# Kernel tuning notes

Hardware: AMD Instinct MI355X
Metric: run time of the kernel (lower is better)

The kernel has to match this reference:

```python
import jax, jax.numpy as jnp
import numpy as np
from jax import lax

B, T, H, W, C = 2, 16, 64, 64, 64
KT, K = 3, 3


def kernel_to_freq_3d(kernel, T, H, W):
    # kernel: (C, k_t, k_h, k_w) -> (C, T, H, W) complex freq response
    Cc, k_t, k_h, k_w = kernel.shape
    t_idx = (jnp.arange(k_t) - k_t // 2) % T
    h_idx = (jnp.arange(k_h) - k_h // 2) % H
    w_idx = (jnp.arange(k_w) - k_w // 2) % W
    tt, th, tw = jnp.meshgrid(t_idx, h_idx, w_idx, indexing='ij')
    padded = jnp.zeros((Cc, T, H, W), dtype=kernel.dtype).at[:, tt, th, tw].set(kernel)
    return jnp.fft.fftn(padded, axes=(1, 2, 3))


def mamba_op(left, right):
    a1, b1 = left
    a2, b2 = right
    return (a1 * a2, a2 * b1 + b2)


def setup_inputs() -> dict:
    key = jax.random.key(0)
    ks = jax.random.split(key, 8)
    fan_in = KT * K * K
    x = jax.random.normal(ks[0], (B, T, H, W, C), dtype=jnp.float32)
    A_kernel = jax.random.normal(ks[1], (C, KT, K, K), dtype=jnp.float32) / np.sqrt(fan_in)
    B_kernel = jax.random.normal(ks[2], (C, KT, K, K), dtype=jnp.float32) / np.sqrt(fan_in)
    forget_bias = jnp.full((C,), 2.0, dtype=jnp.float32)
    forget_scale = jnp.full((C,), 0.01, dtype=jnp.float32)
    input_bias = jnp.zeros((C,), dtype=jnp.float32)
    input_scale = jnp.full((C,), 0.01, dtype=jnp.float32)
    delta_W = jax.random.normal(ks[3], (C, C), dtype=jnp.float32) / np.sqrt(C)
    delta_b = jnp.zeros((C,), dtype=jnp.float32)
    return {"x": x, "A_kernel": A_kernel, "B_kernel": B_kernel,
            "forget_bias": forget_bias, "forget_scale": forget_scale,
            "input_bias": input_bias, "input_scale": input_scale,
            "delta_W": delta_W, "delta_b": delta_b}


def reference(x, A_kernel, B_kernel, forget_bias, forget_scale,
              input_bias, input_scale, delta_W, delta_b):
    Bb, Tt, Hh, Ww, Cc = x.shape
    # freq-domain kernels: (C,T,H,W) -> (T,1,H,W,C) for broadcasting over batch
    A_f = kernel_to_freq_3d(A_kernel, Tt, Hh, Ww).transpose(1, 2, 3, 0)[:, None]
    B_f = kernel_to_freq_3d(B_kernel, Tt, Hh, Ww).transpose(1, 2, 3, 0)[:, None]
    # input-dependent gates (real, elementwise per channel)
    forget_gate = jax.nn.sigmoid(forget_bias + forget_scale * x)
    input_gate = jax.nn.sigmoid(input_bias + input_scale * x)
    delta = jax.nn.softplus(jnp.einsum('bthwc,cd->bthwd', x, delta_W) + delta_b)
    x_f = jnp.fft.fftn(x, axes=(1, 2, 3))  # complex (B,T,H,W,C)
    # move time axis to front for the scan: (T,B,H,W,C)
    a_seq = forget_gate.transpose(1, 0, 2, 3, 4) * A_f
    b_seq = (input_gate.transpose(1, 0, 2, 3, 4)
             * delta.transpose(1, 0, 2, 3, 4)
             * B_f * x_f.transpose(1, 0, 2, 3, 4))
    _, h_all_f = lax.associative_scan(mamba_op, (a_seq, b_seq), axis=0)
    h_f = h_all_f.transpose(1, 0, 2, 3, 4)
    h = jnp.fft.ifftn(h_f, axes=(1, 2, 3)).real
    return h.astype(x.dtype)
```

## Files before the change

### kernel.cpp

```cpp
#include <hip/hip_runtime.h>
#include <math.h>

#define Bb 2
#define Tt 16
#define Hh 64
#define Ww 64
#define Cc 64
#define ST_ (Hh*Ww*Cc)
#define SB_ (Tt*Hh*Ww*Cc)

#define TWO_PI 6.2831853071795864769f

typedef __attribute__((ext_vector_type(8))) short bf16x8;
typedef __attribute__((ext_vector_type(4))) float f32x4;

#define BUF_A    0u
#define BUF_B    8388608u

__device__ __forceinline__ float2 cmul(float2 a, float2 b) {
    return make_float2(fmaf(a.x, b.x, -a.y * b.y), fmaf(a.x, b.y, a.y * b.x));
}
__device__ __forceinline__ float2 cadd(float2 a, float2 b) { return make_float2(a.x + b.x, a.y + b.y); }
__device__ __forceinline__ float2 csub(float2 a, float2 b) { return make_float2(a.x - b.x, a.y - b.y); }

__device__ __forceinline__ unsigned bfpack(float2 f) {
    unsigned r = __float_as_uint(f.x);
    unsigned i = __float_as_uint(f.y);
    r = (r + 0x7fffu + ((r >> 16) & 1u)) >> 16;
    i = (i + 0x7fffu + ((i >> 16) & 1u)) >> 16;
    return r | (i << 16);
}
__device__ __forceinline__ float2 bfunpack(unsigned u) {
    return make_float2(__uint_as_float(u << 16), __uint_as_float(u & 0xffff0000u));
}

union U48 { uint4 u4; uint2 u2[2]; unsigned u[4]; bf16x8 v8; };

__device__ __forceinline__ U48 tw_wf(int wp, int q, int ka, int reim) {
    U48 o;
#pragma unroll
    for (int p = 0; p < 4; ++p) {
        int k0 = ka * 32 + q * 8 + 2 * p;
        float v[2];
#pragma unroll
        for (int dk = 0; dk < 2; ++dk) {
            int k = k0 + dk;
            int a = (wp * k) & 63;
            float sn, cs; sincosf(TWO_PI * (float)a * (1.0f / 64.0f), &sn, &cs);
            v[dk] = reim ? -sn : cs;
        }
        o.u[p] = bfpack(make_float2(v[0], v[1]));
    }
    return o;
}

__device__ __forceinline__ U48 tw_cpx(int wp, int q, int ka, int reim, int tbl) {
    U48 o;
#pragma unroll
    for (int p = 0; p < 4; ++p) {
        int k0 = ka * 32 + q * 8 + 2 * p;
        float v[2];
#pragma unroll
        for (int dk = 0; dk < 2; ++dk) {
            int k = k0 + dk;
            int h = k >> 1;
            int a = (wp * h) & 63;
            float sn, cs; sincosf(TWO_PI * (float)a * (1.0f / 64.0f), &sn, &cs);
            bool even = (k & 1) == 0;
            float vv;
            if (tbl == 1) vv = reim ? (even ? -sn : cs) : (even ? cs : sn);
            else          vv = (reim ? (even ? sn : cs) : (even ? cs : -sn)) * (1.0f / 64.0f);
            v[dk] = vv;
        }
        o.u[p] = bfpack(make_float2(v[0], v[1]));
    }
    return o;
}

__device__ __forceinline__ U48 tw_wi(int wp, int q, int ka) {
    U48 o;
#pragma unroll
    for (int p = 0; p < 4; ++p) {
        int k0 = ka * 32 + q * 8 + 2 * p;
        float v[2];
#pragma unroll
        for (int dk = 0; dk < 2; ++dk) {
            int k = k0 + dk;
            int h = k >> 1;
            int a = (wp * h) & 63;
            float sn, cs; sincosf(TWO_PI * (float)a * (1.0f / 64.0f), &sn, &cs);
            bool even = (k & 1) == 0;
            v[dk] = (even ? cs : -sn) * (1.0f / 64.0f);
        }
        o.u[p] = bfpack(make_float2(v[0], v[1]));
    }
    return o;
}

__device__ __forceinline__ int zidx(int col, int h) {
    return (col << 6) + (h ^ (((col >> 1) & 7) << 3));
}

template <int S>
__device__ __forceinline__ void fft4(float2& a, float2& b, float2& c, float2& d) {
    float2 t0 = cadd(a, c), t1 = csub(a, c);
    float2 t2 = cadd(b, d), t3 = csub(b, d);
    a = cadd(t0, t2);
    c = csub(t0, t2);
    b = make_float2(t1.x - (float)S * t3.y, t1.y + (float)S * t3.x);
    d = make_float2(t1.x + (float)S * t3.y, t1.y - (float)S * t3.x);
}

template <int S>
__device__ __forceinline__ void fft16(float2 v[16]) {
    const float CS[10] = {1.f, 0.92387953f, 0.70710678f, 0.38268343f, 0.f,
                          -0.38268343f, -0.70710678f, -0.92387953f, -1.f, -0.92387953f};
    const float SN[10] = {0.f, 0.38268343f, 0.70710678f, 0.92387953f, 1.f,
                          0.92387953f, 0.70710678f, 0.38268343f, 0.f, -0.38268343f};
    float2 A[4][4];
#pragma unroll
    for (int j = 0; j < 4; ++j) {
        A[j][0] = v[j]; A[j][1] = v[4 + j]; A[j][2] = v[8 + j]; A[j][3] = v[12 + j];
        fft4<S>(A[j][0], A[j][1], A[j][2], A[j][3]);
#pragma unroll
        for (int k0 = 0; k0 < 4; ++k0) {
            int m = j * k0;
            float2 tw = make_float2(CS[m], (float)S * SN[m]);
            A[j][k0] = cmul(A[j][k0], tw);
        }
    }
#pragma unroll
    for (int k0 = 0; k0 < 4; ++k0) {
        fft4<S>(A[0][k0], A[1][k0], A[2][k0], A[3][k0]);
        v[k0] = A[0][k0]; v[k0 + 4] = A[1][k0]; v[k0 + 8] = A[2][k0]; v[k0 + 12] = A[3][k0];
    }
}

__global__ __launch_bounds__(512) void k_fwd2d(const float* __restrict__ x,
                                               unsigned* __restrict__ X2) {
    __shared__ unsigned Z[512 * 64];
    int tid = threadIdx.x;
    int lane = tid & 63, r = (tid >> 6) & 3, team = tid >> 8;
    int m = lane & 15, q = lane >> 4;
    int wg = blockIdx.x;
    int bt = wg >> 3;
    int c0 = (wg & 7) * 8;
    int b = wg >> 7, t = (wg >> 3) & 15;
    const float* xs = x + (size_t)bt * 262144;
    int wp = r * 16 + m;
    int hme = m >> 3, cme = m & 7;

    U48 Are[2], Aim[2];
#pragma unroll
    for (int ka = 0; ka < 2; ++ka) { Are[ka] = tw_wf(wp, q, ka, 0); Aim[ka] = tw_wf(wp, q, ka, 1); }
#pragma unroll 2
    for (int gi = 0; gi < 16; ++gi) {
        int g = gi * 2 + team;
        int h = g * 2 + hme;
        const float* xr = xs + (size_t)h * 4096 + (c0 + cme);
        U48 B[2];
#pragma unroll
        for (int ka = 0; ka < 2; ++ka)
#pragma unroll
            for (int p = 0; p < 4; ++p) {
                int w0 = ka * 32 + q * 8 + 2 * p;
                B[ka].u[p] = bfpack(make_float2(xr[(size_t)w0 * 64], xr[(size_t)(w0 + 1) * 64]));
            }
        f32x4 ar = {0.f, 0.f, 0.f, 0.f}, ai = {0.f, 0.f, 0.f, 0.f};
#pragma unroll
        for (int ka = 0; ka < 2; ++ka) {
            ar = __builtin_amdgcn_mfma_f32_16x16x32_bf16(Are[ka].v8, B[ka].v8, ar, 0, 0, 0);
            ai = __builtin_amdgcn_mfma_f32_16x16x32_bf16(Aim[ka].v8, B[ka].v8, ai, 0, 0, 0);
        }
#pragma unroll
        for (int reg = 0; reg < 4; ++reg) {
            int wpp = r * 16 + q * 4 + reg;
            Z[zidx(wpp * 8 + cme, h)] = bfpack(make_float2(ar[reg], ai[reg]));
        }
    }
    __syncthreads();

    U48 Hre[4], Him[4];
#pragma unroll
    for (int ka = 0; ka < 4; ++ka) { Hre[ka] = tw_cpx(wp, q, ka, 0, 1); Him[ka] = tw_cpx(wp, q, ka, 1, 1); }
    size_t ob = (size_t)b * 4194304 + (size_t)t * 64 + (c0 + cme);
#pragma unroll 2
    for (int gi = 0; gi < 16; ++gi) {
        int g = gi * 2 + team;
        int col = g * 16 + m;
        int w = g * 2 + hme;
        U48 B[4];
#pragma unroll
        for (int ka = 0; ka < 4; ++ka) {
            int h0 = ka * 16 + q * 4;
            int zi = zidx(col, h0);
            B[ka].u2[0] = *(const uint2*)&Z[zi];
            B[ka].u2[1] = *(const uint2*)&Z[zi + 2];
        }
        f32x4 ar = {0.f, 0.f, 0.f, 0.f}, ai = {0.f, 0.f, 0.f, 0.f};
#pragma unroll
        for (int ka = 0; ka < 4; ++ka) {
            ar = __builtin_amdgcn_mfma_f32_16x16x32_bf16(Hre[ka].v8, B[ka].v8, ar, 0, 0, 0);
            ai = __builtin_amdgcn_mfma_f32_16x16x32_bf16(Him[ka].v8, B[ka].v8, ai, 0, 0, 0);
        }
#pragma unroll
        for (int reg = 0; reg < 4; ++reg) {
            int hp = r * 16 + q * 4 + reg;
            X2[ob + (size_t)hp * 65536 + (size_t)w * 1024] = bfpack(make_float2(ar[reg], ai[reg]));
        }
    }
}

__global__ __launch_bounds__(512) void k_inv2d(const unsigned* __restrict__ X3,
                                               float* __restrict__ out) {
    __shared__ unsigned Z[512 * 64];
    int tid = threadIdx.x;
    int lane = tid & 63, r = (tid >> 6) & 3, team = tid >> 8;
    int m = lane & 15, q = lane >> 4;
    int wg = blockIdx.x;
    int bt = wg >> 3;
    int c0 = (wg & 7) * 8;
    const unsigned* xs = X3 + (size_t)bt * 262144;
    int wp = r * 16 + m;
    int hme = m >> 3, cme = m & 7;

    U48 Hre[4], Him[4];
#pragma unroll
    for (int ka = 0; ka < 4; ++ka) { Hre[ka] = tw_cpx(wp, q, ka, 0, 2); Him[ka] = tw_cpx(wp, q, ka, 1, 2); }
#pragma unroll 2
    for (int gi = 0; gi < 16; ++gi) {
        int g = gi * 2 + team;
        int w = g * 2 + hme;
        const unsigned* xr = xs + (size_t)w * 4096 + (c0 + cme);
        U48 B[4];
#pragma unroll
        for (int ka = 0; ka < 4; ++ka)
#pragma unroll
            for (int j = 0; j < 4; ++j) {
                int h = ka * 16 + q * 4 + j;
                B[ka].u[j] = xr[(size_t)h * 64];
            }
        f32x4 ar = {0.f, 0.f, 0.f, 0.f}, ai = {0.f, 0.f, 0.f, 0.f};
#pragma unroll
        for (int ka = 0; ka < 4; ++ka) {
            ar = __builtin_amdgcn_mfma_f32_16x16x32_bf16(Hre[ka].v8, B[ka].v8, ar, 0, 0, 0);
            ai = __builtin_amdgcn_mfma_f32_16x16x32_bf16(Him[ka].v8, B[ka].v8, ai, 0, 0, 0);
        }
#pragma unroll
        for (int reg = 0; reg < 4; ++reg) {
            int hp = r * 16 + q * 4 + reg;
            Z[zidx(hp * 8 + cme, w)] = bfpack(make_float2(ar[reg], ai[reg]));
        }
    }
    __syncthreads();

    U48 Wre[4];
#pragma unroll
    for (int ka = 0; ka < 4; ++ka) Wre[ka] = tw_wi(wp, q, ka);
#pragma unroll 2
    for (int gi = 0; gi < 16; ++gi) {
        int g = gi * 2 + team;
        int col = g * 16 + m;
        int h = g * 2 + hme;
        U48 B[4];
#pragma unroll
        for (int ka = 0; ka < 4; ++ka) {
            int w0 = ka * 16 + q * 4;
            int zi = zidx(col, w0);
            B[ka].u2[0] = *(const uint2*)&Z[zi];
            B[ka].u2[1] = *(const uint2*)&Z[zi + 2];
        }
        f32x4 ar = {0.f, 0.f, 0.f, 0.f};
#pragma unroll
        for (int ka = 0; ka < 4; ++ka)
            ar = __builtin_amdgcn_mfma_f32_16x16x32_bf16(Wre[ka].v8, B[ka].v8, ar, 0, 0, 0);
        float* dst = out + (size_t)bt * 262144 + (size_t)h * 4096 + (c0 + cme);
#pragma unroll
        for (int reg = 0; reg < 4; ++reg) {
            int wpp = r * 16 + q * 4 + reg;
            dst[(size_t)wpp * 64] = ar[reg];
        }
    }
}

__global__ __launch_bounds__(256) void k_mid(
    const float* __restrict__ x, const unsigned* __restrict__ X2,
    unsigned* __restrict__ X3,
    const float* __restrict__ Ak, const float* __restrict__ Bk,
    const float* __restrict__ fb, const float* __restrict__ fs,
    const float* __restrict__ ib, const float* __restrict__ isc_,
    const float* __restrict__ dW, const float* __restrict__ db) {
    const float CT[16] = {1.f, 0.9238795f, 0.7071068f, 0.3826834f, 0.f, -0.3826834f,
                          -0.7071068f, -0.9238795f, -1.f, -0.9238795f, -0.7071068f,
                          -0.3826834f, 0.f, 0.3826834f, 0.7071068f, 0.9238795f};
    const float SN[16] = {0.f, 0.3826834f, 0.7071068f, 0.9238795f, 1.f, 0.9238795f,
                          0.7071068f, 0.3826834f, 0.f, -0.3826834f, -0.7071068f,
                          -0.9238795f, -1.f, -0.9238795f, -0.7071068f, -0.3826834f};
    __shared__ float Akl[1728], Bkl[1728];
    __shared__ __align__(16) float xs[4][16 * 68 + 4];

    int tid = threadIdx.x;
    int g = tid >> 6, lane = tid & 63;
    int c = lane;
    int m = lane & 15, q = lane >> 4;
    int site = blockIdx.x * 4 + g;
    int b = site >> 12, hw = site & 4095;
    int h = hw >> 6, w = hw & 63;
    size_t base = (size_t)b * SB_ + (size_t)hw * 64;

    for (int i = tid; i < 1728; i += 256) { Akl[i] = Ak[i]; Bkl[i] = Bk[i]; }

    U48 Ub[4][2];
#pragma unroll
    for (int nt = 0; nt < 4; ++nt)
#pragma unroll
        for (int ka = 0; ka < 2; ++ka)
#pragma unroll
            for (int p2 = 0; p2 < 4; ++p2) {
                int kb = ka * 32 + q * 8 + 2 * p2;
                int ccol = m + 16 * nt;
                Ub[nt][ka].u[p2] = bfpack(make_float2(dW[kb * 64 + ccol], dW[(kb + 1) * 64 + ccol]));
            }

    float xv[16];
    float2 v[16];
    const unsigned* src2 = X2 + (size_t)site * 1024;
#pragma unroll
    for (int t = 0; t < 16; ++t) {
        xv[t] = x[base + (size_t)t * ST_ + c];
        v[t] = bfunpack(src2[t * 64 + c]);
    }
#pragma unroll
    for (int t = 0; t < 16; ++t) xs[g][t * 68 + c] = xv[t];
    __syncthreads();

    bf16x8 Afrag[2];
#pragma unroll
    for (int ka = 0; ka < 2; ++ka) {
        int d0 = ka * 32 + q * 8;
        const float* p = &xs[g][m * 68 + d0];
        float4 f0 = *(const float4*)p;
        float4 f1 = *(const float4*)(p + 4);
        union { bf16x8 v8; unsigned uu[4]; } U;
        U.uu[0] = bfpack(make_float2(f0.x, f0.y));
        U.uu[1] = bfpack(make_float2(f0.z, f0.w));
        U.uu[2] = bfpack(make_float2(f1.x, f1.y));
        U.uu[3] = bfpack(make_float2(f1.z, f1.w));
        Afrag[ka] = U.v8;
    }
#pragma unroll
    for (int nt = 0; nt < 4; ++nt) {
        int ccol = m + 16 * nt;
        float dbn = db[ccol];
        f32x4 acc = {dbn, dbn, dbn, dbn};
#pragma unroll
        for (int ka = 0; ka < 2; ++ka)
            acc = __builtin_amdgcn_mfma_f32_16x16x32_bf16(Afrag[ka], Ub[nt][ka].v8, acc, 0, 0, 0);
#pragma unroll
        for (int reg = 0; reg < 4; ++reg)
            xs[g][(q * 4 + reg) * 68 + ccol] = acc[reg];
    }

    float sh, ch; sincosf(TWO_PI * (float)h / 64.0f, &sh, &ch);
    float sw, cw; sincosf(TWO_PI * (float)w / 64.0f, &sw, &cw);
    float2 eh[3] = { make_float2(ch, sh), make_float2(1.f, 0.f), make_float2(ch, -sh) };
    float2 ew[3] = { make_float2(cw, sw), make_float2(1.f, 0.f), make_float2(cw, -sw) };
    float2 GA[3], GB[3];
#pragma unroll
    for (int kt = 0; kt < 3; ++kt) { GA[kt] = make_float2(0.f, 0.f); GB[kt] = make_float2(0.f, 0.f); }
#pragma unroll
    for (int kh = 0; kh < 3; ++kh) {
#pragma unroll
        for (int kw = 0; kw < 3; ++kw) {
            float2 e = cmul(eh[kh], ew[kw]);
#pragma unroll
            for (int kt = 0; kt < 3; ++kt) {
                float ka = Akl[c * 27 + kt * 9 + kh * 3 + kw];
                float kb = Bkl[c * 27 + kt * 9 + kh * 3 + kw];
                GA[kt].x = fmaf(ka, e.x, GA[kt].x);
                GA[kt].y = fmaf(ka, e.y, GA[kt].y);
                GB[kt].x = fmaf(kb, e.x, GB[kt].x);
                GB[kt].y = fmaf(kb, e.y, GB[kt].y);
            }
        }
    }
    float fbc = fb[c], fsc = fs[c], ibc = ib[c], iscv = isc_[c];

    fft16<-1>(v);
    __syncthreads();

    float delta_raw[16];
#pragma unroll
    for (int t = 0; t < 16; ++t) delta_raw[t] = xs[g][t * 68 + c];

    float2 hv = make_float2(0.f, 0.f);
#pragma unroll
    for (int t = 0; t < 16; ++t) {
        float ct = CT[t], st = SN[t];
        float2 Af, Bf;
        Af.x = GA[1].x + ct * (GA[0].x + GA[2].x) - st * (GA[0].y - GA[2].y);
        Af.y = GA[1].y + ct * (GA[0].y + GA[2].y) + st * (GA[0].x - GA[2].x);
        Bf.x = GB[1].x + ct * (GB[0].x + GB[2].x) - st * (GB[0].y - GB[2].y);
        Bf.y = GB[1].y + ct * (GB[0].y + GB[2].y) + st * (GB[0].x - GB[2].x);

        float xc = xv[t];
        float fg  = __builtin_amdgcn_rcpf(1.f + __expf(-(fbc + fsc * xc)));
        float igv = __builtin_amdgcn_rcpf(1.f + __expf(-(ibc + iscv * xc)));
        float dot = delta_raw[t];
        float delta = (dot > 20.f) ? dot : __logf(1.f + __expf(dot));

        float sR = igv * delta;
        float2 bbv;
        bbv.x = sR * (Bf.x * v[t].x - Bf.y * v[t].y);
        bbv.y = sR * (Bf.x * v[t].y + Bf.y * v[t].x);
        float2 av = make_float2(fg * Af.x, fg * Af.y);
        float2 nh;
        nh.x = av.x * hv.x - av.y * hv.y + bbv.x;
        nh.y = av.x * hv.y + av.y * hv.x + bbv.y;
        hv = nh;
        v[t] = hv;
    }

    fft16<1>(v);

    size_t ob = (size_t)b * 4194304 + (size_t)w * 4096 + (size_t)h * 64 + c;
#pragma unroll
    for (int t = 0; t < 16; ++t) {
        float2 o = make_float2(v[t].x * 0.0625f, v[t].y * 0.0625f);
        X3[ob + (size_t)t * 262144] = bfpack(o);
    }
}

extern "C" void kernel_launch(void* const* d_in, const int* in_sizes, int n_in,
                              void* d_out, int out_size, void* d_ws, size_t ws_size,
                              hipStream_t stream) {
    const float* x   = (const float*)d_in[0];
    const float* Ak  = (const float*)d_in[1];
    const float* Bk  = (const float*)d_in[2];
    const float* fb  = (const float*)d_in[3];
    const float* fs  = (const float*)d_in[4];
    const float* ib  = (const float*)d_in[5];
    const float* is_ = (const float*)d_in[6];
    const float* dW  = (const float*)d_in[7];
    const float* db  = (const float*)d_in[8];
    float* out = (float*)d_out;
    unsigned* ws = (unsigned*)d_ws;
    unsigned* X2 = ws + BUF_A;
    unsigned* X3 = ws + BUF_B;

    k_fwd2d<<<Bb * Tt * 8, 512, 0, stream>>>(x, X2);
    k_mid<<<(Bb * Hh * Ww) / 4, 256, 0, stream>>>(x, X2, X3, Ak, Bk, fb, fs, ib, is_, dW, db);
    k_inv2d<<<Bb * Tt * 8, 512, 0, stream>>>(X3, out);
}
```

Baseline: 202.0 us.

## Stage first-pass FFT inputs through swizzled LDS with vectorized global loads

In both the forward and inverse 2D FFT kernels, the first MFMA pass used to gather its operands with strided scalar global loads, one channel element per lane. It now loads chunks of rows with float4/uint4 coalesced reads into a small XOR-swizzled shared buffer. The MFMA B operands are then read from that buffer as 128-bit LDS loads. This removes uncoalesced global accesses, at the cost of extra LDS space and more __syncthreads per chunk, which may lower occupancy.

```diff
diff --git a/kernel.cpp b/kernel.cpp
--- a/kernel.cpp
+++ b/kernel.cpp
@@ -139,8 +139,10 @@
 __global__ __launch_bounds__(512) void k_fwd2d(const float* __restrict__ x,
                                                unsigned* __restrict__ X2) {
     __shared__ unsigned Z[512 * 64];
+    __shared__ unsigned P[8 * 16 * 32];
     int tid = threadIdx.x;
     int lane = tid & 63, r = (tid >> 6) & 3, team = tid >> 8;
+    int wv = tid >> 6;
     int m = lane & 15, q = lane >> 4;
     int wg = blockIdx.x;
     int bt = wg >> 3;
@@ -153,32 +155,59 @@
     U48 Are[2], Aim[2];
 #pragma unroll
     for (int ka = 0; ka < 2; ++ka) { Are[ka] = tw_wf(wp, q, ka, 0); Aim[ka] = tw_wf(wp, q, ka, 1); }
-#pragma unroll 2
-    for (int gi = 0; gi < 16; ++gi) {
-        int g = gi * 2 + team;
-        int h = g * 2 + hme;
-        const float* xr = xs + (size_t)h * 4096 + (c0 + cme);
-        U48 B[2];
-#pragma unroll
-        for (int ka = 0; ka < 2; ++ka)
-#pragma unroll
-            for (int p = 0; p < 4; ++p) {
-                int w0 = ka * 32 + q * 8 + 2 * p;
-                B[ka].u[p] = bfpack(make_float2(xr[(size_t)w0 * 64], xr[(size_t)(w0 + 1) * 64]));
-            }
-        f32x4 ar = {0.f, 0.f, 0.f, 0.f}, ai = {0.f, 0.f, 0.f, 0.f};
-#pragma unroll
-        for (int ka = 0; ka < 2; ++ka) {
-            ar = __builtin_amdgcn_mfma_f32_16x16x32_bf16(Are[ka].v8, B[ka].v8, ar, 0, 0, 0);
-            ai = __builtin_amdgcn_mfma_f32_16x16x32_bf16(Aim[ka].v8, B[ka].v8, ai, 0, 0, 0);
-        }
-#pragma unroll
-        for (int reg = 0; reg < 4; ++reg) {
-            int wpp = r * 16 + q * 4 + reg;
-            Z[zidx(wpp * 8 + cme, h)] = bfpack(make_float2(ar[reg], ai[reg]));
-        }
-    }
-    __syncthreads();
+
+    int s_hl = lane >> 4;
+    int s_p  = (lane >> 1) & 7;
+    int s_cq = lane & 1;
+    int s_hb = wv & 3;
+    int s_wh = wv >> 2;
+
+    for (int ch = 0; ch < 4; ++ch) {
+        int hloc = s_hb * 4 + s_hl;
+        int h = ch * 16 + hloc;
+#pragma unroll
+        for (int st = 0; st < 2; ++st) {
+            int w2 = s_wh * 16 + st * 8 + s_p;
+            const float* pa = xs + (size_t)h * 4096 + (size_t)w2 * 128 + (c0 + s_cq * 4);
+            float4 f0 = *(const float4*)pa;
+            float4 f1 = *(const float4*)(pa + 64);
+            float a0[4] = {f0.x, f0.y, f0.z, f0.w};
+            float a1[4] = {f1.x, f1.y, f1.z, f1.w};
+            int hb3 = h & 3;
+#pragma unroll
+            for (int j = 0; j < 4; ++j) {
+                int c = s_cq * 4 + j;
+                int w2s = w2 ^ ((hb3 ^ ((c & 1) << 1)) << 3);
+                P[c * 512 + hloc * 32 + w2s] = bfpack(make_float2(a0[j], a1[j]));
+            }
+        }
+        __syncthreads();
+#pragma unroll
+        for (int gi = 0; gi < 4; ++gi) {
+            int g = ch * 8 + gi * 2 + team;
+            int h2 = g * 2 + hme;
+            int hl2 = h2 & 15;
+            int swz = ((h2 & 3) ^ ((cme & 1) << 1)) << 3;
+            U48 B[2];
+#pragma unroll
+            for (int ka = 0; ka < 2; ++ka) {
+                int w2a = (ka * 16 + q * 4) ^ swz;
+                B[ka].u4 = *(const uint4*)&P[cme * 512 + hl2 * 32 + w2a];
+            }
+            f32x4 ar = {0.f, 0.f, 0.f, 0.f}, ai = {0.f, 0.f, 0.f, 0.f};
+#pragma unroll
+            for (int ka = 0; ka < 2; ++ka) {
+                ar = __builtin_amdgcn_mfma_f32_16x16x32_bf16(Are[ka].v8, B[ka].v8, ar, 0, 0, 0);
+                ai = __builtin_amdgcn_mfma_f32_16x16x32_bf16(Aim[ka].v8, B[ka].v8, ai, 0, 0, 0);
+            }
+#pragma unroll
+            for (int reg = 0; reg < 4; ++reg) {
+                int wpp = r * 16 + q * 4 + reg;
+                Z[zidx(wpp * 8 + cme, h2)] = bfpack(make_float2(ar[reg], ai[reg]));
+            }
+        }
+        __syncthreads();
+    }
 
     U48 Hre[4], Him[4];
 #pragma unroll
@@ -214,6 +243,7 @@
 __global__ __launch_bounds__(512) void k_inv2d(const unsigned* __restrict__ X3,
                                                float* __restrict__ out) {
     __shared__ unsigned Z[512 * 64];
+    __shared__ unsigned P[8 * 8 * 64];
     int tid = threadIdx.x;
     int lane = tid & 63, r = (tid >> 6) & 3, team = tid >> 8;
     int m = lane & 15, q = lane >> 4;
@@ -227,32 +257,49 @@
     U48 Hre[4], Him[4];
 #pragma unroll
     for (int ka = 0; ka < 4; ++ka) { Hre[ka] = tw_cpx(wp, q, ka, 0, 2); Him[ka] = tw_cpx(wp, q, ka, 1, 2); }
-#pragma unroll 2
-    for (int gi = 0; gi < 16; ++gi) {
-        int g = gi * 2 + team;
-        int w = g * 2 + hme;
-        const unsigned* xr = xs + (size_t)w * 4096 + (c0 + cme);
-        U48 B[4];
-#pragma unroll
-        for (int ka = 0; ka < 4; ++ka)
+
+    for (int cw = 0; cw < 8; ++cw) {
+#pragma unroll
+        for (int it = 0; it < 2; ++it) {
+            int u = it * 512 + tid;
+            int cq = u & 1, h = (u >> 1) & 63, wl = u >> 7;
+            const unsigned* pa = xs + (size_t)(cw * 8 + wl) * 4096 + (size_t)h * 64 + (c0 + cq * 4);
+            uint4 d = *(const uint4*)pa;
+            unsigned dd[4] = {d.x, d.y, d.z, d.w};
 #pragma unroll
             for (int j = 0; j < 4; ++j) {
-                int h = ka * 16 + q * 4 + j;
-                B[ka].u[j] = xr[(size_t)h * 64];
-            }
-        f32x4 ar = {0.f, 0.f, 0.f, 0.f}, ai = {0.f, 0.f, 0.f, 0.f};
-#pragma unroll
-        for (int ka = 0; ka < 4; ++ka) {
-            ar = __builtin_amdgcn_mfma_f32_16x16x32_bf16(Hre[ka].v8, B[ka].v8, ar, 0, 0, 0);
-            ai = __builtin_amdgcn_mfma_f32_16x16x32_bf16(Him[ka].v8, B[ka].v8, ai, 0, 0, 0);
-        }
-#pragma unroll
-        for (int reg = 0; reg < 4; ++reg) {
-            int hp = r * 16 + q * 4 + reg;
-            Z[zidx(hp * 8 + cme, w)] = bfpack(make_float2(ar[reg], ai[reg]));
-        }
-    }
-    __syncthreads();
+                int c = cq * 4 + j;
+                int hs = h ^ ((((wl & 3) ^ ((c & 1) << 1))) << 3);
+                P[c * 512 + wl * 64 + hs] = dd[j];
+            }
+        }
+        __syncthreads();
+#pragma unroll
+        for (int gi = 0; gi < 2; ++gi) {
+            int g = cw * 4 + gi * 2 + team;
+            int w = g * 2 + hme;
+            int wl = w & 7;
+            int swz = ((wl & 3) ^ ((cme & 1) << 1)) << 3;
+            U48 B[4];
+#pragma unroll
+            for (int ka = 0; ka < 4; ++ka) {
+                int ha = (ka * 16 + q * 4) ^ swz;
+                B[ka].u4 = *(const uint4*)&P[cme * 512 + wl * 64 + ha];
+            }
+            f32x4 ar = {0.f, 0.f, 0.f, 0.f}, ai = {0.f, 0.f, 0.f, 0.f};
+#pragma unroll
+            for (int ka = 0; ka < 4; ++ka) {
+                ar = __builtin_amdgcn_mfma_f32_16x16x32_bf16(Hre[ka].v8, B[ka].v8, ar, 0, 0, 0);
+                ai = __builtin_amdgcn_mfma_f32_16x16x32_bf16(Him[ka].v8, B[ka].v8, ai, 0, 0, 0);
+            }
+#pragma unroll
+            for (int reg = 0; reg < 4; ++reg) {
+                int hp = r * 16 + q * 4 + reg;
+                Z[zidx(hp * 8 + cme, w)] = bfpack(make_float2(ar[reg], ai[reg]));
+            }
+        }
+        __syncthreads();
+    }
 
     U48 Wre[4];
 #pragma unroll
```

Result: faster. 197.6 us (-2.1%).
